# Kernel tuning notes

Measured on AMD Instinct MI355X. Metric: run time of the kernel, lower is better.

Reference implementation:

```python
import jax, jax.numpy as jnp
import numpy as np

MARGIN = 0.3
N = 8192
D = 128
NUM_CLASSES = 256

def setup_inputs() -> dict:
    key = jax.random.key(0)
    k1, k2 = jax.random.split(key)
    inputs = jax.random.normal(k1, (N, D), dtype=jnp.float32)
    targets = jax.random.randint(k2, (N,), 0, NUM_CLASSES, dtype=jnp.int64)
    return {"inputs": inputs, "targets": targets}

def reference(inputs, targets):
    n = inputs.shape[0]
    dt = inputs.dtype
    # pairwise euclidean distances: ||xi||^2 + ||xj||^2 - 2 xi.xj, clamped and sqrt'ed
    sq = jnp.sum(inputs * inputs, axis=1)                     # [n]
    d2 = sq[:, None] + sq[None, :] - 2.0 * (inputs @ inputs.T)
    dist = jnp.sqrt(jnp.clip(d2, 1e-12, None))                # [n, n]
    dsq = dist * dist                                         # squared dists used by the loss

    mask = targets[:, None] == targets[None, :]               # same-identity mask [n, n]

    # positives: torch code sorts and drops the smallest (the self-distance ~1e-6)
    pos_d = jnp.where(mask, dist, jnp.inf)
    min_idx = jnp.argmin(pos_d, axis=1)                       # index of dropped element per row
    excl = jnp.arange(n)[None, :] == min_idx[:, None]
    pos_valid = mask & ~excl                                  # remaining positives
    cnt_p = jnp.sum(pos_valid, axis=1).astype(dt)
    sigma_p = jnp.sum(jnp.where(pos_valid, dsq, 0.0), axis=1) / cnt_p
    max_p = jnp.max(jnp.where(pos_valid, dsq, -jnp.inf), axis=1)
    dist_ap = max_p / sigma_p + 0.5 * jnp.log(sigma_p)        # [n]

    # negatives: all different-identity entries
    neg = ~mask
    cnt_n = jnp.sum(neg, axis=1).astype(dt)
    sigma_n = jnp.sum(jnp.where(neg, dsq, 0.0), axis=1) / cnt_n
    min_n = jnp.min(jnp.where(neg, dsq, jnp.inf), axis=1)
    dist_an = min_n / sigma_n + 0.5 * jnp.log(sigma_n)        # [n]

    # MarginRankingLoss with y=1: mean(max(0, -(an - ap) + margin))
    loss = jnp.mean(jnp.maximum(dist_ap - dist_an + MARGIN, 0.0))
    return loss
```

## Files before the change

kernel.cpp:

```cpp
#include <hip/hip_runtime.h>
#include <math.h>


#define NROWS 8192
#define MARGIN_F 0.3f

typedef short bf16x8 __attribute__((ext_vector_type(8)));
typedef float f32x16 __attribute__((ext_vector_type(16)));
union U4B { uint4 u; bf16x8 h; };

__device__ __forceinline__ unsigned short f2bf(float x) {
    unsigned u = __float_as_uint(x);
    return (unsigned short)((u + 0x7fffu + ((u >> 16) & 1u)) >> 16);
}

__global__ __launch_bounds__(256) void prep_kernel(const float* __restrict__ X,
                                                   const int* __restrict__ tgt,
                                                   float* __restrict__ sq,
                                                   float* __restrict__ upk,
                                                   unsigned short* __restrict__ Xbf,
                                                   int* __restrict__ hist,
                                                   float* __restrict__ S_class,
                                                   float* __restrict__ bsum) {
    int tid = threadIdx.x, w = tid >> 6, l = tid & 63;
    int row0 = blockIdx.x * 32 + w * 8;
    float rs = 0.0f;
    #pragma unroll
    for (int i = 0; i < 8; ++i) {
        int r = row0 + i;
        float2 v = ((const float2*)X)[(size_t)r * 64 + l];
        ushort2 h2;
        h2.x = f2bf(v.x);
        h2.y = f2bf(v.y);
        ((ushort2*)Xbf)[(size_t)r * 64 + l] = h2;
        float s = v.x * v.x + v.y * v.y;
        for (int d = 32; d > 0; d >>= 1) s += __shfl_down(s, d, 64);
        if (l == 0) {
            sq[r] = s;
            rs += s;
            int c = tgt[r];
            upk[r] = __uint_as_float((__float_as_uint(0.5f * s) & 0xffffff00u) | (unsigned)c);
            atomicAdd(&hist[c], 1);
            atomicAdd(&S_class[c], s);
        }
    }
    __shared__ float bs[4];
    if (l == 0) bs[w] = rs;
    __syncthreads();
    if (tid == 0) bsum[blockIdx.x] = bs[0] + bs[1] + bs[2] + bs[3];
}

__global__ __launch_bounds__(256, 3) void dist_kernel(
        const unsigned short* __restrict__ Xbf, const int* __restrict__ tgt,
        const float* __restrict__ upk, float4* __restrict__ partial,
        int ns_mask, int jb_shift, int tiles) {
    __shared__ uint4 As[128 * 16];
    __shared__ float ush[128];
    const int tid = threadIdx.x;
    const int w = tid >> 6, l = tid & 63, hl = l >> 5, l31 = l & 31;
    const int bx = blockIdx.x;
    const int slice = bx & ns_mask;
    const int jb = bx >> jb_shift;

    {
        const uint4* src = (const uint4*)Xbf + (size_t)jb * 64 * 16;
        #pragma unroll
        for (int s = 0; s < 4; ++s) {
            int g = s * 256 + tid, row = g >> 4, c = g & 15;
            As[row * 16 + (c ^ (row & 15))] = src[g];
        }
    }
    __syncthreads();
    bf16x8 Bf[2][8];
    int tjt[2];
    #pragma unroll
    for (int ct = 0; ct < 2; ++ct) {
        int colb = ct * 32 + l31;
        tjt[ct] = tgt[jb * 64 + colb];
        #pragma unroll
        for (int kk = 0; kk < 8; ++kk) {
            U4B t; t.u = As[colb * 16 + ((kk * 2 + hl) ^ (colb & 15))];
            Bf[ct][kk] = t.h;
        }
    }

    float Sa[2] = {0.f, 0.f};
    float Ss[2] = {0.f, 0.f};
    float Mp[2] = {-INFINITY, -INFINITY};
    float Mn[2] = { INFINITY,  INFINITY};

    for (int t = 0; t < tiles; ++t) {
        const int i0 = (slice * tiles + t) * 128;
        __syncthreads();
        {
            const uint4* src = (const uint4*)Xbf + (size_t)i0 * 16;
            #pragma unroll
            for (int s = 0; s < 8; ++s) {
                int g = s * 256 + tid, row = g >> 4, c = g & 15;
                As[row * 16 + (c ^ (row & 15))] = src[g];
            }
            if (tid < 128) ush[tid] = upk[i0 + tid];
        }
        __syncthreads();

        float ur[16];
        #pragma unroll
        for (int r = 0; r < 16; ++r)
            ur[r] = ush[w * 32 + (r & 3) + 8 * (r >> 2) + 4 * hl];

        f32x16 acc[2];
        acc[0] = (f32x16)0.0f;
        acc[1] = (f32x16)0.0f;
        const int arow = w * 32 + l31;
        #pragma unroll
        for (int kk = 0; kk < 8; ++kk) {
            U4B a; a.u = As[arow * 16 + ((kk * 2 + hl) ^ (arow & 15))];
            acc[0] = __builtin_amdgcn_mfma_f32_32x32x16_bf16(a.h, Bf[0][kk], acc[0], 0, 0, 0);
            acc[1] = __builtin_amdgcn_mfma_f32_32x32x16_bf16(a.h, Bf[1][kk], acc[1], 0, 0, 0);
        }

        #pragma unroll
        for (int ct = 0; ct < 2; ++ct) {
            const int tt = tjt[ct];
            #pragma unroll
            for (int r = 0; r < 16; ++r) {
                float a = acc[ct][r];
                float v = ur[r] - a;
                bool same = ((__float_as_int(ur[r]) & 0xff) == tt);
                Sa[ct] += a;
                Ss[ct] += same ? a : 0.0f;
                Mp[ct] = fmaxf(Mp[ct], same ? v : -INFINITY);
                Mn[ct] = same ? Mn[ct] : fminf(Mn[ct], v);
            }
        }
    }

    #pragma unroll
    for (int ct = 0; ct < 2; ++ct) {
        Sa[ct] += __shfl_xor(Sa[ct], 32, 64);
        Ss[ct] += __shfl_xor(Ss[ct], 32, 64);
        Mp[ct] = fmaxf(Mp[ct], __shfl_xor(Mp[ct], 32, 64));
        Mn[ct] = fminf(Mn[ct], __shfl_xor(Mn[ct], 32, 64));
    }
    __syncthreads();
    float4* sm = (float4*)As;
    if (l < 32) {
        #pragma unroll
        for (int ct = 0; ct < 2; ++ct)
            sm[(ct * 32 + l31) * 4 + w] = make_float4(Sa[ct], Ss[ct], Mp[ct], Mn[ct]);
    }
    __syncthreads();
    if (tid < 64) {
        float4 a = sm[tid * 4 + 0], b = sm[tid * 4 + 1];
        float4 c2 = sm[tid * 4 + 2], d = sm[tid * 4 + 3];
        float4 o;
        o.x = a.x + b.x + c2.x + d.x;
        o.y = a.y + b.y + c2.y + d.y;
        o.z = fmaxf(fmaxf(a.z, b.z), fmaxf(c2.z, d.z));
        o.w = fminf(fminf(a.w, b.w), fminf(c2.w, d.w));
        partial[(size_t)slice * NROWS + jb * 64 + tid] = o;
    }
}

__global__ __launch_bounds__(256) void combine_kernel(
        const float* __restrict__ sq, const int* __restrict__ tgt,
        const int* __restrict__ hist, const float* __restrict__ S_class,
        const float* __restrict__ bsum, const float4* __restrict__ partial,
        float* __restrict__ blocksum, int ns) {
    __shared__ float red[4];
    __shared__ float hs[4];
    int tid = threadIdx.x, l = tid & 63, w = tid >> 6;

    float b = bsum[tid];
    for (int d = 32; d > 0; d >>= 1) b += __shfl_down(b, d, 64);
    if (l == 0) red[w] = b;
    __syncthreads();
    float S_all = red[0] + red[1] + red[2] + red[3];

    int j = blockIdx.x * 256 + tid;
    float Sa = 0.f, Ss = 0.f, Mp = -INFINITY, Mn = INFINITY;
    for (int s = 0; s < ns; ++s) {
        float4 p = partial[(size_t)s * NROWS + j];
        Sa += p.x; Ss += p.y;
        Mp = fmaxf(Mp, p.z); Mn = fminf(Mn, p.w);
    }
    float sqj = sq[j];
    int c = tgt[j];
    float cnt = (float)hist[c];
    float sumall = (float)NROWS * sqj + S_all - 2.0f * Sa;
    float sump = cnt * sqj + S_class[c] - 2.0f * Ss;
    float sumn = sumall - sump;
    float sigp = sump / (cnt - 1.0f);
    float sign_ = sumn / ((float)NROWS - cnt);
    float ap = (sqj + 2.0f * Mp) / sigp + 0.5f * __logf(sigp);
    float an = (sqj + 2.0f * Mn) / sign_ + 0.5f * __logf(sign_);
    float h = fmaxf(ap - an + MARGIN_F, 0.0f);
    for (int d = 32; d > 0; d >>= 1) h += __shfl_down(h, d, 64);
    if (l == 0) hs[w] = h;
    __syncthreads();
    if (tid == 0) blocksum[blockIdx.x] = hs[0] + hs[1] + hs[2] + hs[3];
}

__global__ __launch_bounds__(64) void final_kernel(const float* __restrict__ blocksum,
                                                   float* __restrict__ out) {
    int tid = threadIdx.x;
    float s = (tid < 32) ? blocksum[tid] : 0.0f;
    for (int d = 32; d > 0; d >>= 1) s += __shfl_down(s, d, 64);
    if (tid == 0) out[0] = s * (1.0f / NROWS);
}

extern "C" void kernel_launch(void* const* d_in, const int* in_sizes, int n_in,
                              void* d_out, int out_size, void* d_ws, size_t ws_size,
                              hipStream_t stream) {
    const float* X = (const float*)d_in[0];
    const int* tgt = (const int*)d_in[1];
    float* out = (float*)d_out;

    float* f = (float*)d_ws;
    int*   hist     = (int*)f;
    float* S_class  = f + 256;
    float* bsum     = f + 512;
    float* blocksum = f + 768;
    float* sq       = f + 1024;
    float* upk      = f + 9216;
    unsigned short* Xbf = (unsigned short*)(f + 17408);
    float4* partial = (float4*)(f + 541696);

    int ns = 16;
    while (ns > 2 && ws_size < ((size_t)541696 + (size_t)ns * NROWS * 4) * sizeof(float))
        ns >>= 1;
    int shift = (ns == 16) ? 4 : (ns == 8) ? 3 : 2;
    int tiles = 64 / ns;

    hipMemsetAsync(d_ws, 0, 2048, stream);
    prep_kernel<<<256, 256, 0, stream>>>(X, tgt, sq, upk, Xbf, hist, S_class, bsum);
    dist_kernel<<<128 * ns, 256, 0, stream>>>(Xbf, tgt, upk, partial,
                                              ns - 1, shift, tiles);
    combine_kernel<<<32, 256, 0, stream>>>(sq, tgt, hist, S_class, bsum,
                                           partial, blocksum, ns);
    final_kernel<<<1, 64, 0, stream>>>(blocksum, out);
}
```

Baseline: 119.1 us.

## Sort rows by class so tiles outside the class range skip mask logic

Adds a histogram kernel and a scan kernel, then counting-sorts rows by class inside the prep kernel: squared norms, packed labels and the bf16 rows are scattered to class-sorted positions. With that ordering, each distance block knows which row range shares classes with its 64 columns, and tiles outside that range use a cheaper epilogue that tracks only the total sum and the negative minimum. Separately, the distance kernel drops LDS staging and reads A/B fragments and labels straight from global memory into registers, removing the block barriers. The cost is two extra small launches, atomic-ordered scatter writes, and uncoalesced-looking 16-byte global loads that now depend on L2 hits instead of shared memory.

```diff
diff --git a/kernel.cpp b/kernel.cpp
--- a/kernel.cpp
+++ b/kernel.cpp
@@ -12,6 +12,34 @@
 __device__ __forceinline__ unsigned short f2bf(float x) {
     unsigned u = __float_as_uint(x);
     return (unsigned short)((u + 0x7fffu + ((u >> 16) & 1u)) >> 16);
+}
+
+__global__ __launch_bounds__(256) void hist_kernel(const int* __restrict__ tgt,
+                                                   int* __restrict__ hist) {
+    int i = blockIdx.x * 256 + threadIdx.x;
+    atomicAdd(&hist[tgt[i]], 1);
+}
+
+__global__ __launch_bounds__(256) void scan_kernel(const int* __restrict__ hist,
+                                                   int* __restrict__ cstart,
+                                                   int* __restrict__ coffset) {
+    int t = threadIdx.x;
+    int h = hist[t];
+    int x = h;
+    #pragma unroll
+    for (int d = 1; d < 64; d <<= 1) {
+        int y = __shfl_up(x, d, 64);
+        if ((t & 63) >= d) x += y;
+    }
+    __shared__ int wsum[4];
+    if ((t & 63) == 63) wsum[t >> 6] = x;
+    __syncthreads();
+    int off = 0;
+    for (int i = 0; i < (t >> 6); ++i) off += wsum[i];
+    int excl = off + x - h;
+    cstart[t] = excl;
+    coffset[t] = excl;
+    if (t == 255) cstart[256] = NROWS;
 }
 
 __global__ __launch_bounds__(256) void prep_kernel(const float* __restrict__ X,
@@ -19,7 +47,7 @@
                                                    float* __restrict__ sq,
                                                    float* __restrict__ upk,
                                                    unsigned short* __restrict__ Xbf,
-                                                   int* __restrict__ hist,
+                                                   int* __restrict__ coffset,
                                                    float* __restrict__ S_class,
                                                    float* __restrict__ bsum) {
     int tid = threadIdx.x, w = tid >> 6, l = tid & 63;
@@ -32,17 +60,19 @@
         ushort2 h2;
         h2.x = f2bf(v.x);
         h2.y = f2bf(v.y);
-        ((ushort2*)Xbf)[(size_t)r * 64 + l] = h2;
         float s = v.x * v.x + v.y * v.y;
         for (int d = 32; d > 0; d >>= 1) s += __shfl_down(s, d, 64);
+        int pos = 0;
         if (l == 0) {
-            sq[r] = s;
+            int c = tgt[r];
+            pos = atomicAdd(&coffset[c], 1);
+            sq[pos] = s;
             rs += s;
-            int c = tgt[r];
-            upk[r] = __uint_as_float((__float_as_uint(0.5f * s) & 0xffffff00u) | (unsigned)c);
-            atomicAdd(&hist[c], 1);
+            upk[pos] = __uint_as_float((__float_as_uint(0.5f * s) & 0xffffff00u) | (unsigned)c);
             atomicAdd(&S_class[c], s);
         }
+        pos = __shfl(pos, 0, 64);
+        ((ushort2*)Xbf)[(size_t)pos * 64 + l] = h2;
     }
     __shared__ float bs[4];
     if (l == 0) bs[w] = rs;
@@ -51,38 +81,33 @@
 }
 
 __global__ __launch_bounds__(256, 3) void dist_kernel(
-        const unsigned short* __restrict__ Xbf, const int* __restrict__ tgt,
-        const float* __restrict__ upk, float4* __restrict__ partial,
+        const unsigned short* __restrict__ Xbf, const float* __restrict__ upk,
+        const int* __restrict__ cstart, float4* __restrict__ partial,
         int ns_mask, int jb_shift, int tiles) {
-    __shared__ uint4 As[128 * 16];
-    __shared__ float ush[128];
     const int tid = threadIdx.x;
     const int w = tid >> 6, l = tid & 63, hl = l >> 5, l31 = l & 31;
     const int bx = blockIdx.x;
     const int slice = bx & ns_mask;
     const int jb = bx >> jb_shift;
-
-    {
-        const uint4* src = (const uint4*)Xbf + (size_t)jb * 64 * 16;
-        #pragma unroll
-        for (int s = 0; s < 4; ++s) {
-            int g = s * 256 + tid, row = g >> 4, c = g & 15;
-            As[row * 16 + (c ^ (row & 15))] = src[g];
-        }
-    }
-    __syncthreads();
+    const int col0 = jb * 64;
+
     bf16x8 Bf[2][8];
     int tjt[2];
     #pragma unroll
     for (int ct = 0; ct < 2; ++ct) {
-        int colb = ct * 32 + l31;
-        tjt[ct] = tgt[jb * 64 + colb];
+        int colb = col0 + ct * 32 + l31;
+        tjt[ct] = __float_as_int(upk[colb]) & 0xff;
+        const uint4* brow = (const uint4*)Xbf + (size_t)colb * 16;
         #pragma unroll
         for (int kk = 0; kk < 8; ++kk) {
-            U4B t; t.u = As[colb * 16 + ((kk * 2 + hl) ^ (colb & 15))];
+            U4B t; t.u = brow[kk * 2 + hl];
             Bf[ct][kk] = t.h;
         }
     }
+    const int c_first = __float_as_int(upk[col0]) & 0xff;
+    const int c_last  = __float_as_int(upk[col0 + 63]) & 0xff;
+    const int U0 = cstart[c_first];
+    const int U1 = cstart[c_last + 1];
 
     float Sa[2] = {0.f, 0.f};
     float Ss[2] = {0.f, 0.f};
@@ -91,46 +116,51 @@
 
     for (int t = 0; t < tiles; ++t) {
         const int i0 = (slice * tiles + t) * 128;
-        __syncthreads();
-        {
-            const uint4* src = (const uint4*)Xbf + (size_t)i0 * 16;
-            #pragma unroll
-            for (int s = 0; s < 8; ++s) {
-                int g = s * 256 + tid, row = g >> 4, c = g & 15;
-                As[row * 16 + (c ^ (row & 15))] = src[g];
-            }
-            if (tid < 128) ush[tid] = upk[i0 + tid];
-        }
-        __syncthreads();
+        const uint4* ap = (const uint4*)Xbf + (size_t)(i0 + w * 32 + l31) * 16;
+        const float4* up = (const float4*)(upk + i0 + w * 32 + 4 * hl);
 
         float ur[16];
         #pragma unroll
-        for (int r = 0; r < 16; ++r)
-            ur[r] = ush[w * 32 + (r & 3) + 8 * (r >> 2) + 4 * hl];
+        for (int g = 0; g < 4; ++g) {
+            float4 u4 = up[g * 2];
+            ur[g * 4 + 0] = u4.x; ur[g * 4 + 1] = u4.y;
+            ur[g * 4 + 2] = u4.z; ur[g * 4 + 3] = u4.w;
+        }
 
         f32x16 acc[2];
         acc[0] = (f32x16)0.0f;
         acc[1] = (f32x16)0.0f;
-        const int arow = w * 32 + l31;
         #pragma unroll
         for (int kk = 0; kk < 8; ++kk) {
-            U4B a; a.u = As[arow * 16 + ((kk * 2 + hl) ^ (arow & 15))];
+            U4B a; a.u = ap[kk * 2 + hl];
             acc[0] = __builtin_amdgcn_mfma_f32_32x32x16_bf16(a.h, Bf[0][kk], acc[0], 0, 0, 0);
             acc[1] = __builtin_amdgcn_mfma_f32_32x32x16_bf16(a.h, Bf[1][kk], acc[1], 0, 0, 0);
         }
 
-        #pragma unroll
-        for (int ct = 0; ct < 2; ++ct) {
-            const int tt = tjt[ct];
+        if (i0 < U1 && i0 + 128 > U0) {
             #pragma unroll
-            for (int r = 0; r < 16; ++r) {
-                float a = acc[ct][r];
-                float v = ur[r] - a;
-                bool same = ((__float_as_int(ur[r]) & 0xff) == tt);
-                Sa[ct] += a;
-                Ss[ct] += same ? a : 0.0f;
-                Mp[ct] = fmaxf(Mp[ct], same ? v : -INFINITY);
-                Mn[ct] = same ? Mn[ct] : fminf(Mn[ct], v);
+            for (int ct = 0; ct < 2; ++ct) {
+                const int tt = tjt[ct];
+                #pragma unroll
+                for (int r = 0; r < 16; ++r) {
+                    float a = acc[ct][r];
+                    float v = ur[r] - a;
+                    bool same = ((__float_as_int(ur[r]) & 0xff) == tt);
+                    Sa[ct] += a;
+                    Ss[ct] += same ? a : 0.0f;
+                    Mp[ct] = fmaxf(Mp[ct], same ? v : -INFINITY);
+                    Mn[ct] = same ? Mn[ct] : fminf(Mn[ct], v);
+                }
+            }
+        } else {
+            #pragma unroll
+            for (int ct = 0; ct < 2; ++ct) {
+                #pragma unroll
+                for (int r = 0; r < 16; ++r) {
+                    float a = acc[ct][r];
+                    Sa[ct] += a;
+                    Mn[ct] = fminf(Mn[ct], ur[r] - a);
+                }
             }
         }
     }
@@ -142,8 +172,7 @@
         Mp[ct] = fmaxf(Mp[ct], __shfl_xor(Mp[ct], 32, 64));
         Mn[ct] = fminf(Mn[ct], __shfl_xor(Mn[ct], 32, 64));
     }
-    __syncthreads();
-    float4* sm = (float4*)As;
+    __shared__ float4 sm[64 * 4];
     if (l < 32) {
         #pragma unroll
         for (int ct = 0; ct < 2; ++ct)
@@ -158,12 +187,12 @@
         o.y = a.y + b.y + c2.y + d.y;
         o.z = fmaxf(fmaxf(a.z, b.z), fmaxf(c2.z, d.z));
         o.w = fminf(fminf(a.w, b.w), fminf(c2.w, d.w));
-        partial[(size_t)slice * NROWS + jb * 64 + tid] = o;
+        partial[(size_t)slice * NROWS + col0 + tid] = o;
     }
 }
 
 __global__ __launch_bounds__(256) void combine_kernel(
-        const float* __restrict__ sq, const int* __restrict__ tgt,
+        const float* __restrict__ sq, const float* __restrict__ upk,
         const int* __restrict__ hist, const float* __restrict__ S_class,
         const float* __restrict__ bsum, const float4* __restrict__ partial,
         float* __restrict__ blocksum, int ns) {
@@ -185,7 +214,7 @@
         Mp = fmaxf(Mp, p.z); Mn = fminf(Mn, p.w);
     }
     float sqj = sq[j];
-    int c = tgt[j];
+    int c = __float_as_int(upk[j]) & 0xff;
     float cnt = (float)hist[c];
     float sumall = (float)NROWS * sqj + S_all - 2.0f * Sa;
     float sump = cnt * sqj + S_class[c] - 2.0f * Ss;
@@ -221,22 +250,26 @@
     float* S_class  = f + 256;
     float* bsum     = f + 512;
     float* blocksum = f + 768;
-    float* sq       = f + 1024;
-    float* upk      = f + 9216;
-    unsigned short* Xbf = (unsigned short*)(f + 17408);
-    float4* partial = (float4*)(f + 541696);
+    int*   cstart   = (int*)(f + 800);
+    int*   coffset  = (int*)(f + 1088);
+    float* sq       = f + 2048;
+    float* upk      = f + 10240;
+    unsigned short* Xbf = (unsigned short*)(f + 18432);
+    float4* partial = (float4*)(f + 542720);
 
     int ns = 16;
-    while (ns > 2 && ws_size < ((size_t)541696 + (size_t)ns * NROWS * 4) * sizeof(float))
+    while (ns > 2 && ws_size < ((size_t)542720 + (size_t)ns * NROWS * 4) * sizeof(float))
         ns >>= 1;
     int shift = (ns == 16) ? 4 : (ns == 8) ? 3 : 2;
     int tiles = 64 / ns;
 
     hipMemsetAsync(d_ws, 0, 2048, stream);
-    prep_kernel<<<256, 256, 0, stream>>>(X, tgt, sq, upk, Xbf, hist, S_class, bsum);
-    dist_kernel<<<128 * ns, 256, 0, stream>>>(Xbf, tgt, upk, partial,
+    hist_kernel<<<32, 256, 0, stream>>>(tgt, hist);
+    scan_kernel<<<1, 256, 0, stream>>>(hist, cstart, coffset);
+    prep_kernel<<<256, 256, 0, stream>>>(X, tgt, sq, upk, Xbf, coffset, S_class, bsum);
+    dist_kernel<<<128 * ns, 256, 0, stream>>>(Xbf, upk, cstart, partial,
                                               ns - 1, shift, tiles);
-    combine_kernel<<<32, 256, 0, stream>>>(sq, tgt, hist, S_class, bsum,
+    combine_kernel<<<32, 256, 0, stream>>>(sq, upk, hist, S_class, bsum,
                                            partial, blocksum, ns);
     final_kernel<<<1, 64, 0, stream>>>(blocksum, out);
 }
```

Result: slower. 148.2 us (+24.4%).
